# Optimization experiments

Measured on AMD Instinct MI355X. Metric: run time of the kernel, lower is better.

The kernel has to match this reference:

```python
import jax, jax.numpy as jnp
import numpy as np


def _layernorm(x, g, b, eps=1e-5):
    mu = jnp.mean(x, axis=-1, keepdims=True)
    var = jnp.mean(jnp.square(x - mu), axis=-1, keepdims=True)
    return (x - mu) * jax.lax.rsqrt(var + eps) * g + b


def setup_inputs() -> dict:
    key = jax.random.key(0)
    ks = jax.random.split(key, 8)
    B, S, E, K, H = 32, 64, 768, 36, 4
    w = 0.02
    return {
        "x": jax.random.normal(ks[0], (B, S, E), dtype=jnp.float32),
        "y": jax.random.normal(ks[1], (B * S, K, E), dtype=jnp.float32),
        "ln_gamma": jnp.ones((H, E), jnp.float32),
        "ln_beta": jnp.zeros((H, E), jnp.float32),
        "W1": jax.random.normal(ks[2], (H, E, E), dtype=jnp.float32) * w,
        "b1": jnp.zeros((H, E), jnp.float32),
        "W2x": jax.random.normal(ks[3], (H, E), dtype=jnp.float32) * w,  # first half of Linear(2E,1)
        "W2y": jax.random.normal(ks[4], (H, E), dtype=jnp.float32) * w,  # second half of Linear(2E,1)
        "b2": jnp.zeros((H,), jnp.float32),
        "Wm": jax.random.normal(ks[5], (H * E, E), dtype=jnp.float32) * w,
        "bm": jnp.zeros((E,), jnp.float32),
        "select_indegree_num": 36,
    }


def reference(x, y, ln_gamma, ln_beta, W1, b1, W2x, W2y, b2, Wm, bm, select_indegree_num):
    # x: [B,S,E], y: [B*S,K,E]; dropout layers are identity in eval mode.
    B, S, E = x.shape
    H = ln_gamma.shape[0]
    xf = x.reshape(B * S, E)
    outs = []
    for h in range(H):
        # shared linear1 (LayerNorm + Linear) applied to both x and y
        x_ = _layernorm(xf, ln_gamma[h], ln_beta[h]) @ W1[h] + b1[h]          # [BS,E]
        y_ = _layernorm(y, ln_gamma[h], ln_beta[h]) @ W1[h] + b1[h]           # [BS,K,E]
        logit = (x_ @ W2x[h])[:, None] + y_ @ W2y[h] + b2[h]                  # [BS,K]
        prob = jax.nn.softmax(logit, axis=1)                                   # softmax over neighbors
        a = jnp.einsum('nk,nke->ne', prob, y_)                                 # weighted sum, [BS,E]
        outs.append(jax.nn.gelu(xf + a))                                       # GELU(x + a)
    cat = jnp.concatenate(outs, axis=-1)                                       # [BS,H*E]
    res = jax.nn.gelu(cat @ Wm + bm).reshape(B, S, E)
    return x + res  # has_residual=True
```

## Files before the change

### kernel.cpp

```cpp
#include <hip/hip_runtime.h>
#include <hip/hip_bf16.h>
#include <math.h>

#define EE 768
#define HH 4
#define KK 36
#define BSN 2048

typedef __attribute__((ext_vector_type(8))) short short8;
typedef __attribute__((ext_vector_type(4))) short short4v;
typedef __attribute__((ext_vector_type(4))) float float4v;

__device__ inline short f2bf(float x){
  return __builtin_bit_cast(short, __float2bfloat16(x));
}
__device__ inline float bf2f(short s){
  return __bfloat162float(__builtin_bit_cast(__hip_bfloat16, s));
}
__device__ inline float gelu_tanh(float x){
  float t = tanhf(0.79788456080286536f * (x + 0.044715f * x * x * x));
  return 0.5f * x * (1.0f + t);
}

__global__ __launch_bounds__(256) void k_v(const float* __restrict__ W1,
                                           const float* __restrict__ W2y,
                                           const float* __restrict__ g,
                                           const float* __restrict__ b1,
                                           float* __restrict__ v,
                                           float* __restrict__ b1p){
  const int wid  = blockIdx.x * 4 + (threadIdx.x >> 6);
  const int lane = threadIdx.x & 63;
  const int h = wid / EE, e = wid % EE;
  const float* W  = W1 + ((size_t)h * EE + e) * EE;
  const float* wy = W2y + h * EE;
  float acc = 0.f;
  #pragma unroll
  for (int j = 0; j < 12; ++j){
    int f = lane + 64 * j;
    acc += W[f] * wy[f];
  }
  #pragma unroll
  for (int off = 32; off; off >>= 1) acc += __shfl_xor(acc, off);
  if (lane == 0) v[h * EE + e] = g[h * EE + e] * acc;

  int idx = blockIdx.x * 256 + threadIdx.x;
  if (idx < HH * EE) b1p[idx] = b1[idx];
}

__global__ __launch_bounds__(256) void k_b1p_acc(const float* __restrict__ W1,
                                                 const float* __restrict__ beta,
                                                 float* __restrict__ b1p){
  const int h   = blockIdx.x >> 6;
  const int ec0 = (blockIdx.x & 63) * 12;
  const float* W  = W1 + (size_t)h * EE * EE;
  const float* bt = beta + h * EE;
  const int f = threadIdx.x;
  float a0 = 0.f, a1 = 0.f, a2 = 0.f;
  #pragma unroll
  for (int e = ec0; e < ec0 + 12; ++e){
    float be = bt[e];
    const float* row = W + (size_t)e * EE;
    a0 += be * row[f];
    a1 += be * row[f + 256];
    a2 += be * row[f + 512];
  }
  atomicAdd(&b1p[h * EE + f],       a0);
  atomicAdd(&b1p[h * EE + f + 256], a1);
  atomicAdd(&b1p[h * EE + f + 512], a2);
}

__global__ __launch_bounds__(256) void k_tW1(const float* __restrict__ W1,
                                             const float* __restrict__ g,
                                             short* __restrict__ W1t){
  __shared__ float tile[32][33];
  const int h  = blockIdx.z;
  const int e0 = blockIdx.x * 32, f0 = blockIdx.y * 32;
  const int tx = threadIdx.x & 31, ty = threadIdx.x >> 5;
  const float* W = W1 + (size_t)h * EE * EE;
  #pragma unroll
  for (int i = 0; i < 4; ++i){
    int e = e0 + ty + 8 * i;
    tile[ty + 8 * i][tx] = W[(size_t)e * EE + f0 + tx] * g[h * EE + e];
  }
  __syncthreads();
  #pragma unroll
  for (int i = 0; i < 4; ++i){
    int f = f0 + ty + 8 * i;
    W1t[((size_t)h * EE + f) * EE + e0 + tx] = f2bf(tile[tx][ty + 8 * i]);
  }
}

__global__ __launch_bounds__(256) void k_tWm(const float* __restrict__ Wm,
                                             short* __restrict__ Wmt){
  __shared__ float tile[32][33];
  const int c0 = blockIdx.x * 32, f0 = blockIdx.y * 32;
  const int tx = threadIdx.x & 31, ty = threadIdx.x >> 5;
  #pragma unroll
  for (int i = 0; i < 4; ++i){
    tile[ty + 8 * i][tx] = Wm[(size_t)(c0 + ty + 8 * i) * EE + f0 + tx];
  }
  __syncthreads();
  #pragma unroll
  for (int i = 0; i < 4; ++i){
    Wmt[(size_t)(f0 + ty + 8 * i) * (HH * EE) + c0 + tx] = f2bf(tile[tx][ty + 8 * i]);
  }
}

__global__ __launch_bounds__(256) void k_pass_y(const float* __restrict__ y,
                                                const float* __restrict__ v,
                                                short* __restrict__ p_y){
  const int wave = threadIdx.x >> 6, lane = threadIdx.x & 63;
  const int n = blockIdx.x * 4 + wave;
  const float* base = y + (size_t)n * KK * EE + 4 * lane;

  float4v vreg[HH][3];
  #pragma unroll
  for (int h = 0; h < HH; ++h)
    #pragma unroll
    for (int j = 0; j < 3; ++j)
      vreg[h][j] = *(const float4v*)(v + h * EE + 4 * lane + 256 * j);

  float4v acc[HH][3];
  #pragma unroll
  for (int h = 0; h < HH; ++h)
    #pragma unroll
    for (int j = 0; j < 3; ++j)
      acc[h][j] = (float4v){0.f, 0.f, 0.f, 0.f};
  float m[HH], l[HH];
  #pragma unroll
  for (int h = 0; h < HH; ++h){ m[h] = -INFINITY; l[h] = 0.f; }

  float4v bufA[3], bufB[3];
  #pragma unroll
  for (int j = 0; j < 3; ++j) bufA[j] = *(const float4v*)(base + 256 * j);
  #pragma unroll
  for (int j = 0; j < 3; ++j) bufB[j] = *(const float4v*)(base + EE + 256 * j);

  #pragma unroll 2
  for (int k = 0; k < KK; ++k){
    float4v cur[3];
    #pragma unroll
    for (int j = 0; j < 3; ++j) cur[j] = bufA[j];
    #pragma unroll
    for (int j = 0; j < 3; ++j) bufA[j] = bufB[j];
    if (k + 2 < KK){
      const float* rp = base + (size_t)(k + 2) * EE;
      #pragma unroll
      for (int j = 0; j < 3; ++j) bufB[j] = *(const float4v*)(rp + 256 * j);
    }

    float s = 0.f, s2 = 0.f;
    #pragma unroll
    for (int j = 0; j < 3; ++j)
      #pragma unroll
      for (int c = 0; c < 4; ++c){ float t = cur[j][c]; s += t; s2 += t * t; }
    #pragma unroll
    for (int off = 32; off; off >>= 1){
      s  += __shfl_xor(s, off);
      s2 += __shfl_xor(s2, off);
    }
    const float mu = s * (1.f / EE);
    const float rs = rsqrtf(s2 * (1.f / EE) - mu * mu + 1e-5f);

    float d[HH] = {0.f, 0.f, 0.f, 0.f};
    #pragma unroll
    for (int j = 0; j < 3; ++j)
      #pragma unroll
      for (int c = 0; c < 4; ++c){
        float t = (cur[j][c] - mu) * rs;
        cur[j][c] = t;
        d[0] += t * vreg[0][j][c];
        d[1] += t * vreg[1][j][c];
        d[2] += t * vreg[2][j][c];
        d[3] += t * vreg[3][j][c];
      }
    #pragma unroll
    for (int off = 32; off; off >>= 1){
      d[0] += __shfl_xor(d[0], off);
      d[1] += __shfl_xor(d[1], off);
      d[2] += __shfl_xor(d[2], off);
      d[3] += __shfl_xor(d[3], off);
    }

    #pragma unroll
    for (int h = 0; h < HH; ++h){
      if (d[h] > m[h]){
        float sc = __expf(m[h] - d[h]);
        l[h] *= sc;
        #pragma unroll
        for (int j = 0; j < 3; ++j)
          #pragma unroll
          for (int c = 0; c < 4; ++c) acc[h][j][c] *= sc;
        m[h] = d[h];
      }
      float w = __expf(d[h] - m[h]);
      l[h] += w;
      #pragma unroll
      for (int j = 0; j < 3; ++j)
        #pragma unroll
        for (int c = 0; c < 4; ++c) acc[h][j][c] += w * cur[j][c];
    }
  }

  #pragma unroll
  for (int h = 0; h < HH; ++h){
    const float inv = 1.f / l[h];
    #pragma unroll
    for (int j = 0; j < 3; ++j){
      short4v pk;
      #pragma unroll
      for (int c = 0; c < 4; ++c) pk[c] = f2bf(acc[h][j][c] * inv);
      *(short4v*)(p_y + ((size_t)h * BSN + n) * EE + 4 * lane + 256 * j) = pk;
    }
  }
}

template<int MODE>
__global__ __launch_bounds__(256) void k_gemm(const short* __restrict__ A,
                                              const short* __restrict__ Bt,
                                              const float* __restrict__ addv,
                                              const float* __restrict__ x,
                                              void* __restrict__ out,
                                              int Kdim, size_t strideA, size_t strideB){
  __shared__ short As[64][72];
  __shared__ short Bs[64][72];
  const int z = blockIdx.z;
  const short* Ah; const short* Bh; int kbeg, kend;
  if (MODE == 0){ Ah = A + strideA * z; Bh = Bt + strideB * z; kbeg = 0; kend = Kdim; }
  else          { Ah = A; Bh = Bt; kbeg = z * (Kdim >> 1); kend = kbeg + (Kdim >> 1); }

  const int tid = threadIdx.x;
  const int wave = tid >> 6, lane = tid & 63;
  const int quad = lane >> 4, l16 = lane & 15;
  const int m0 = blockIdx.x * 64, n0 = blockIdx.y * 64;
  const int r = tid >> 3, c8 = (tid & 7) * 8;

  float4v acc[4];
  #pragma unroll
  for (int t = 0; t < 4; ++t) acc[t] = (float4v){0.f, 0.f, 0.f, 0.f};

  const short* Ap0 = Ah + (size_t)(m0 + r) * Kdim + c8;
  const short* Ap1 = Ah + (size_t)(m0 + r + 32) * Kdim + c8;
  const short* Bp0 = Bh + (size_t)(n0 + r) * Kdim + c8;
  const short* Bp1 = Bh + (size_t)(n0 + r + 32) * Kdim + c8;

  for (int k0 = kbeg; k0 < kend; k0 += 64){
    short8 a0 = *(const short8*)(Ap0 + k0);
    short8 a1 = *(const short8*)(Ap1 + k0);
    short8 b0 = *(const short8*)(Bp0 + k0);
    short8 b1 = *(const short8*)(Bp1 + k0);
    __syncthreads();
    *(short8*)(&As[r][c8])      = a0;
    *(short8*)(&As[r + 32][c8]) = a1;
    *(short8*)(&Bs[r][c8])      = b0;
    *(short8*)(&Bs[r + 32][c8]) = b1;
    __syncthreads();
    #pragma unroll
    for (int kk = 0; kk < 64; kk += 32){
      short8 bf = *(const short8*)(&Bs[16 * wave + l16][kk + quad * 8]);
      #pragma unroll
      for (int t = 0; t < 4; ++t){
        short8 af = *(const short8*)(&As[16 * t + l16][kk + quad * 8]);
        acc[t] = __builtin_amdgcn_mfma_f32_16x16x32_bf16(af, bf, acc[t], 0, 0, 0);
      }
    }
  }

  const int f = n0 + 16 * wave + l16;
  if (MODE == 0){
    const float add = addv[768 * z + f];
    #pragma unroll
    for (int t = 0; t < 4; ++t){
      #pragma unroll
      for (int rr = 0; rr < 4; ++rr){
        const int m = m0 + 16 * t + quad * 4 + rr;
        const float val = acc[t][rr] + add;
        const float xf = x[(size_t)m * EE + f];
        ((short*)out)[(size_t)m * (HH * EE) + 768 * z + f] = f2bf(gelu_tanh(xf + val));
      }
    }
  } else {
    float* po = (float*)out + (size_t)z * BSN * EE;
    #pragma unroll
    for (int t = 0; t < 4; ++t){
      #pragma unroll
      for (int rr = 0; rr < 4; ++rr){
        const int m = m0 + 16 * t + quad * 4 + rr;
        po[(size_t)m * EE + f] = acc[t][rr];
      }
    }
  }
}

__global__ __launch_bounds__(256) void k_ep(const float* __restrict__ part,
                                            const float* __restrict__ bm,
                                            const float* __restrict__ x,
                                            float* __restrict__ out){
  const size_t i = ((size_t)blockIdx.x * 256 + threadIdx.x) * 4;
  float4v p0 = *(const float4v*)(part + i);
  float4v p1 = *(const float4v*)(part + (size_t)BSN * EE + i);
  float4v xv = *(const float4v*)(x + i);
  float4v bv = *(const float4v*)(bm + (int)(i % EE));
  float4v o;
  #pragma unroll
  for (int c = 0; c < 4; ++c) o[c] = xv[c] + gelu_tanh(p0[c] + p1[c] + bv[c]);
  *(float4v*)(out + i) = o;
}

extern "C" void kernel_launch(void* const* d_in, const int* in_sizes, int n_in,
                              void* d_out, int out_size, void* d_ws, size_t ws_size,
                              hipStream_t stream){
  const float* x    = (const float*)d_in[0];
  const float* y    = (const float*)d_in[1];
  const float* g    = (const float*)d_in[2];
  const float* beta = (const float*)d_in[3];
  const float* W1   = (const float*)d_in[4];
  const float* b1   = (const float*)d_in[5];
  const float* W2y  = (const float*)d_in[7];
  const float* Wm   = (const float*)d_in[9];
  const float* bm   = (const float*)d_in[10];

  char* ws = (char*)d_ws;
  float* v    = (float*)(ws + 0);
  float* b1p  = (float*)(ws + 12288);
  short* W1t  = (short*)(ws + 24576);
  short* Wmt  = (short*)(ws + 4743168);
  short* p_y  = (short*)(ws + 9461760);
  short* catb = (short*)(ws + 22044672);
  float* part = (float*)(ws + 34627584);
  float* out  = (float*)d_out;

  k_v<<<dim3(768), dim3(256), 0, stream>>>(W1, W2y, g, b1, v, b1p);
  k_b1p_acc<<<dim3(256), dim3(256), 0, stream>>>(W1, beta, b1p);
  k_tW1<<<dim3(24, 24, 4), dim3(256), 0, stream>>>(W1, g, W1t);
  k_tWm<<<dim3(96, 24), dim3(256), 0, stream>>>(Wm, Wmt);
  k_pass_y<<<dim3(512), dim3(256), 0, stream>>>(y, v, p_y);
  k_gemm<0><<<dim3(32, 12, 4), dim3(256), 0, stream>>>(
      p_y, W1t, b1p, x, (void*)catb, 768, (size_t)2048 * 768, (size_t)768 * 768);
  k_gemm<1><<<dim3(32, 12, 2), dim3(256), 0, stream>>>(
      catb, Wmt, nullptr, nullptr, (void*)part, 3072, (size_t)0, (size_t)0);
  k_ep<<<dim3(1536), dim3(256), 0, stream>>>(part, bm, x, out);
}
```

Before: 429.1 us.

## Use 128x128 MFMA GEMM tiles with direct global-to-LDS loads and 4-way split-K

Both bf16 GEMMs move from 64x64 tiles, where each wave computed 4 MFMA outputs, to 128x128 tiles on a 2x2 wave grid with a 4x4 MFMA accumulator block per wave. This raises arithmetic intensity per LDS and global load. Tiles are staged with global_load_lds instead of going through registers. The output-projection GEMM is split over K into 4 chunks instead of 2 to keep enough blocks in flight, and the epilogue sums four partials. In exchange, the unpadded LDS layout may cause bank conflicts, there is more register pressure, and the partial buffer in the workspace doubles in size.

```diff
diff --git a/kernel.cpp b/kernel.cpp
--- a/kernel.cpp
+++ b/kernel.cpp
@@ -6,6 +6,7 @@
 #define HH 4
 #define KK 36
 #define BSN 2048
+#define SPLITK 4
 
 typedef __attribute__((ext_vector_type(8))) short short8;
 typedef __attribute__((ext_vector_type(4))) short short4v;
@@ -20,6 +21,12 @@
 __device__ inline float gelu_tanh(float x){
   float t = tanhf(0.79788456080286536f * (x + 0.044715f * x * x * x));
   return 0.5f * x * (1.0f + t);
+}
+
+__device__ __forceinline__ void gload16(const short* g, short* l){
+  __builtin_amdgcn_global_load_lds(
+      (const __attribute__((address_space(1))) unsigned int*)g,
+      (__attribute__((address_space(3))) unsigned int*)l, 16, 0, 0);
 }
 
 __global__ __launch_bounds__(256) void k_v(const float* __restrict__ W1,
@@ -216,77 +223,90 @@
 }
 
 template<int MODE>
-__global__ __launch_bounds__(256) void k_gemm(const short* __restrict__ A,
-                                              const short* __restrict__ Bt,
-                                              const float* __restrict__ addv,
-                                              const float* __restrict__ x,
-                                              void* __restrict__ out,
-                                              int Kdim, size_t strideA, size_t strideB){
-  __shared__ short As[64][72];
-  __shared__ short Bs[64][72];
+__global__ __launch_bounds__(256) void k_gemm128(const short* __restrict__ A,
+                                                 const short* __restrict__ Bt,
+                                                 const float* __restrict__ addv,
+                                                 const float* __restrict__ x,
+                                                 void* __restrict__ out,
+                                                 int Kdim, size_t strideA, size_t strideB,
+                                                 int kchunk){
+  __shared__ short As[128 * 64];
+  __shared__ short Bs[128 * 64];
   const int z = blockIdx.z;
   const short* Ah; const short* Bh; int kbeg, kend;
   if (MODE == 0){ Ah = A + strideA * z; Bh = Bt + strideB * z; kbeg = 0; kend = Kdim; }
-  else          { Ah = A; Bh = Bt; kbeg = z * (Kdim >> 1); kend = kbeg + (Kdim >> 1); }
+  else          { Ah = A; Bh = Bt; kbeg = z * kchunk; kend = kbeg + kchunk; }
 
   const int tid = threadIdx.x;
   const int wave = tid >> 6, lane = tid & 63;
+  const int wr = wave >> 1, wc = wave & 1;
   const int quad = lane >> 4, l16 = lane & 15;
-  const int m0 = blockIdx.x * 64, n0 = blockIdx.y * 64;
-  const int r = tid >> 3, c8 = (tid & 7) * 8;
-
-  float4v acc[4];
-  #pragma unroll
-  for (int t = 0; t < 4; ++t) acc[t] = (float4v){0.f, 0.f, 0.f, 0.f};
-
-  const short* Ap0 = Ah + (size_t)(m0 + r) * Kdim + c8;
-  const short* Ap1 = Ah + (size_t)(m0 + r + 32) * Kdim + c8;
-  const short* Bp0 = Bh + (size_t)(n0 + r) * Kdim + c8;
-  const short* Bp1 = Bh + (size_t)(n0 + r + 32) * Kdim + c8;
+  const int m0 = blockIdx.x * 128, n0 = blockIdx.y * 128;
+
+  const int srow = lane >> 3;
+  const int scol = (lane & 7) * 8;
+  const int q0 = wave * 4;
+
+  float4v acc[4][4];
+  #pragma unroll
+  for (int t = 0; t < 4; ++t)
+    #pragma unroll
+    for (int u = 0; u < 4; ++u) acc[t][u] = (float4v){0.f, 0.f, 0.f, 0.f};
 
   for (int k0 = kbeg; k0 < kend; k0 += 64){
-    short8 a0 = *(const short8*)(Ap0 + k0);
-    short8 a1 = *(const short8*)(Ap1 + k0);
-    short8 b0 = *(const short8*)(Bp0 + k0);
-    short8 b1 = *(const short8*)(Bp1 + k0);
     __syncthreads();
-    *(short8*)(&As[r][c8])      = a0;
-    *(short8*)(&As[r + 32][c8]) = a1;
-    *(short8*)(&Bs[r][c8])      = b0;
-    *(short8*)(&Bs[r + 32][c8]) = b1;
+    #pragma unroll
+    for (int i = 0; i < 4; ++i){
+      const int q = q0 + i;
+      gload16(Ah + (size_t)(m0 + 8 * q + srow) * Kdim + k0 + scol, &As[q * 512]);
+      gload16(Bh + (size_t)(n0 + 8 * q + srow) * Kdim + k0 + scol, &Bs[q * 512]);
+    }
     __syncthreads();
     #pragma unroll
     for (int kk = 0; kk < 64; kk += 32){
-      short8 bf = *(const short8*)(&Bs[16 * wave + l16][kk + quad * 8]);
+      short8 bfr[4], afr[4];
+      #pragma unroll
+      for (int u = 0; u < 4; ++u)
+        bfr[u] = *(const short8*)(&Bs[(wc * 64 + 16 * u + l16) * 64 + kk + quad * 8]);
+      #pragma unroll
+      for (int t = 0; t < 4; ++t)
+        afr[t] = *(const short8*)(&As[(wr * 64 + 16 * t + l16) * 64 + kk + quad * 8]);
+      #pragma unroll
+      for (int t = 0; t < 4; ++t)
+        #pragma unroll
+        for (int u = 0; u < 4; ++u)
+          acc[t][u] = __builtin_amdgcn_mfma_f32_16x16x32_bf16(afr[t], bfr[u], acc[t][u], 0, 0, 0);
+    }
+  }
+
+  if (MODE == 0){
+    #pragma unroll
+    for (int u = 0; u < 4; ++u){
+      const int f = n0 + wc * 64 + 16 * u + l16;
+      const float add = addv[768 * z + f];
       #pragma unroll
       for (int t = 0; t < 4; ++t){
-        short8 af = *(const short8*)(&As[16 * t + l16][kk + quad * 8]);
-        acc[t] = __builtin_amdgcn_mfma_f32_16x16x32_bf16(af, bf, acc[t], 0, 0, 0);
-      }
-    }
-  }
-
-  const int f = n0 + 16 * wave + l16;
-  if (MODE == 0){
-    const float add = addv[768 * z + f];
-    #pragma unroll
-    for (int t = 0; t < 4; ++t){
-      #pragma unroll
-      for (int rr = 0; rr < 4; ++rr){
-        const int m = m0 + 16 * t + quad * 4 + rr;
-        const float val = acc[t][rr] + add;
-        const float xf = x[(size_t)m * EE + f];
-        ((short*)out)[(size_t)m * (HH * EE) + 768 * z + f] = f2bf(gelu_tanh(xf + val));
+        #pragma unroll
+        for (int rr = 0; rr < 4; ++rr){
+          const int m = m0 + wr * 64 + 16 * t + quad * 4 + rr;
+          const float val = acc[t][u][rr] + add;
+          const float xf = x[(size_t)m * EE + f];
+          ((short*)out)[(size_t)m * (HH * EE) + 768 * z + f] = f2bf(gelu_tanh(xf + val));
+        }
       }
     }
   } else {
     float* po = (float*)out + (size_t)z * BSN * EE;
     #pragma unroll
-    for (int t = 0; t < 4; ++t){
-      #pragma unroll
-      for (int rr = 0; rr < 4; ++rr){
-        const int m = m0 + 16 * t + quad * 4 + rr;
-        po[(size_t)m * EE + f] = acc[t][rr];
+    for (int u = 0; u < 4; ++u){
+      const int f = n0 + wc * 64 + 16 * u + l16;
+      #pragma unroll
+      for (int t = 0; t < 4; ++t){
+        #pragma unroll
+        for (int rr = 0; rr < 4; ++rr){
+          const int m = m0 + wr * 64 + 16 * t + quad * 4 + rr;
+          po[(size_t)m * EE + f] = acc[t][u][rr];
+        }
       }
     }
   }
@@ -297,13 +317,16 @@
                                             const float* __restrict__ x,
                                             float* __restrict__ out){
   const size_t i = ((size_t)blockIdx.x * 256 + threadIdx.x) * 4;
-  float4v p0 = *(const float4v*)(part + i);
-  float4v p1 = *(const float4v*)(part + (size_t)BSN * EE + i);
+  float4v s0 = *(const float4v*)(part + i);
+  float4v s1 = *(const float4v*)(part + (size_t)BSN * EE + i);
+  float4v s2 = *(const float4v*)(part + (size_t)2 * BSN * EE + i);
+  float4v s3 = *(const float4v*)(part + (size_t)3 * BSN * EE + i);
   float4v xv = *(const float4v*)(x + i);
   float4v bv = *(const float4v*)(bm + (int)(i % EE));
   float4v o;
   #pragma unroll
-  for (int c = 0; c < 4; ++c) o[c] = xv[c] + gelu_tanh(p0[c] + p1[c] + bv[c]);
+  for (int c = 0; c < 4; ++c)
+    o[c] = xv[c] + gelu_tanh(s0[c] + s1[c] + s2[c] + s3[c] + bv[c]);
   *(float4v*)(out + i) = o;
 }
 
@@ -335,9 +358,9 @@
   k_tW1<<<dim3(24, 24, 4), dim3(256), 0, stream>>>(W1, g, W1t);
   k_tWm<<<dim3(96, 24), dim3(256), 0, stream>>>(Wm, Wmt);
   k_pass_y<<<dim3(512), dim3(256), 0, stream>>>(y, v, p_y);
-  k_gemm<0><<<dim3(32, 12, 4), dim3(256), 0, stream>>>(
-      p_y, W1t, b1p, x, (void*)catb, 768, (size_t)2048 * 768, (size_t)768 * 768);
-  k_gemm<1><<<dim3(32, 12, 2), dim3(256), 0, stream>>>(
-      catb, Wmt, nullptr, nullptr, (void*)part, 3072, (size_t)0, (size_t)0);
+  k_gemm128<0><<<dim3(16, 6, 4), dim3(256), 0, stream>>>(
+      p_y, W1t, b1p, x, (void*)catb, 768, (size_t)2048 * 768, (size_t)768 * 768, 0);
+  k_gemm128<1><<<dim3(16, 6, SPLITK), dim3(256), 0, stream>>>(
+      catb, Wmt, nullptr, nullptr, (void*)part, 3072, (size_t)0, (size_t)0, 3072 / SPLITK);
   k_ep<<<dim3(1536), dim3(256), 0, stream>>>(part, bm, x, out);
 }
```

New measurement: 445.1 us. +3.7%, slower.

## Double-buffer LDS tiles in bf16 GEMM with register prefetch

Applied to the files above, without the earlier changes.

Converts the GEMM main loop to ping-pong LDS buffers. The next tile is written to the alternate buffer and the tile after that is prefetched into registers while MFMAs run on the current buffer, leaving one barrier per iteration instead of two. The goal is to hide global load latency and cut barrier stalls, at the cost of twice the shared memory per block, which may lower occupancy.

```diff
diff --git a/kernel.cpp b/kernel.cpp
--- a/kernel.cpp
+++ b/kernel.cpp
@@ -222,8 +222,8 @@
                                               const float* __restrict__ x,
                                               void* __restrict__ out,
                                               int Kdim, size_t strideA, size_t strideB){
-  __shared__ short As[64][72];
-  __shared__ short Bs[64][72];
+  __shared__ short As[2][64][72];
+  __shared__ short Bs[2][64][72];
   const int z = blockIdx.z;
   const short* Ah; const short* Bh; int kbeg, kend;
   if (MODE == 0){ Ah = A + strideA * z; Bh = Bt + strideB * z; kbeg = 0; kend = Kdim; }
@@ -244,26 +244,48 @@
   const short* Bp0 = Bh + (size_t)(n0 + r) * Kdim + c8;
   const short* Bp1 = Bh + (size_t)(n0 + r + 32) * Kdim + c8;
 
+  short8 ra0 = *(const short8*)(Ap0 + kbeg);
+  short8 ra1 = *(const short8*)(Ap1 + kbeg);
+  short8 rb0 = *(const short8*)(Bp0 + kbeg);
+  short8 rb1 = *(const short8*)(Bp1 + kbeg);
+  *(short8*)(&As[0][r][c8])      = ra0;
+  *(short8*)(&As[0][r + 32][c8]) = ra1;
+  *(short8*)(&Bs[0][r][c8])      = rb0;
+  *(short8*)(&Bs[0][r + 32][c8]) = rb1;
+  if (kbeg + 64 < kend){
+    ra0 = *(const short8*)(Ap0 + kbeg + 64);
+    ra1 = *(const short8*)(Ap1 + kbeg + 64);
+    rb0 = *(const short8*)(Bp0 + kbeg + 64);
+    rb1 = *(const short8*)(Bp1 + kbeg + 64);
+  }
+  __syncthreads();
+
+  int cur = 0;
   for (int k0 = kbeg; k0 < kend; k0 += 64){
-    short8 a0 = *(const short8*)(Ap0 + k0);
-    short8 a1 = *(const short8*)(Ap1 + k0);
-    short8 b0 = *(const short8*)(Bp0 + k0);
-    short8 b1 = *(const short8*)(Bp1 + k0);
+    if (k0 + 64 < kend){
+      const int nx = cur ^ 1;
+      *(short8*)(&As[nx][r][c8])      = ra0;
+      *(short8*)(&As[nx][r + 32][c8]) = ra1;
+      *(short8*)(&Bs[nx][r][c8])      = rb0;
+      *(short8*)(&Bs[nx][r + 32][c8]) = rb1;
+      if (k0 + 128 < kend){
+        ra0 = *(const short8*)(Ap0 + k0 + 128);
+        ra1 = *(const short8*)(Ap1 + k0 + 128);
+        rb0 = *(const short8*)(Bp0 + k0 + 128);
+        rb1 = *(const short8*)(Bp1 + k0 + 128);
+      }
+    }
+    #pragma unroll
+    for (int kk = 0; kk < 64; kk += 32){
+      short8 bf = *(const short8*)(&Bs[cur][16 * wave + l16][kk + quad * 8]);
+      #pragma unroll
+      for (int t = 0; t < 4; ++t){
+        short8 af = *(const short8*)(&As[cur][16 * t + l16][kk + quad * 8]);
+        acc[t] = __builtin_amdgcn_mfma_f32_16x16x32_bf16(af, bf, acc[t], 0, 0, 0);
+      }
+    }
     __syncthreads();
-    *(short8*)(&As[r][c8])      = a0;
-    *(short8*)(&As[r + 32][c8]) = a1;
-    *(short8*)(&Bs[r][c8])      = b0;
-    *(short8*)(&Bs[r + 32][c8]) = b1;
-    __syncthreads();
-    #pragma unroll
-    for (int kk = 0; kk < 64; kk += 32){
-      short8 bf = *(const short8*)(&Bs[16 * wave + l16][kk + quad * 8]);
-      #pragma unroll
-      for (int t = 0; t < 4; ++t){
-        short8 af = *(const short8*)(&As[16 * t + l16][kk + quad * 8]);
-        acc[t] = __builtin_amdgcn_mfma_f32_16x16x32_bf16(af, bf, acc[t], 0, 0, 0);
-      }
-    }
+    cur ^= 1;
   }
 
   const int f = n0 + 16 * wave + l16;
```

Measured after the change: 427.4 us. Within noise of the previous version (-0.4%).
